# Performance work log

Hardware: AMD Instinct MI355X
Metric: run time of the kernel (lower is better)

The kernel has to match this reference:

```python
import jax, jax.numpy as jnp
import numpy as np

NUM_AUTHOR = 16604
NUM_PAPER = 12455
NUM_NODES = NUM_AUTHOR + NUM_PAPER  # 29059
EMBED_DIM = 300
B = 32768          # batch of query nodes
E = 1048576        # total neighbor edges (avg degree 32)


def setup_inputs() -> dict:
    key = jax.random.key(0)
    k1, k2, k3, k4, k5, k6 = jax.random.split(key, 6)
    nodes = jax.random.randint(k1, (B,), 0, NUM_NODES)
    seg = jnp.sort(jax.random.randint(k2, (E,), 0, B))
    neighbors = jax.random.randint(k3, (E,), 0, NUM_NODES)
    embeddings = jax.random.normal(k4, (NUM_NODES, EMBED_DIM), dtype=jnp.float32)
    # linear1: Linear(3*300 -> 300)
    lim = 1.0 / np.sqrt(3 * EMBED_DIM)
    W1 = jax.random.uniform(k5, (EMBED_DIM, 3 * EMBED_DIM), dtype=jnp.float32, minval=-lim, maxval=lim)
    b1 = jax.random.uniform(k6, (EMBED_DIM,), dtype=jnp.float32, minval=-lim, maxval=lim)
    return {"nodes": nodes, "seg": seg, "neighbors": neighbors,
            "embeddings": embeddings, "W1": W1, "b1": b1}


def reference(nodes, seg, neighbors, embeddings, W1, b1):
    # Gather neighbor embeddings: [E, D] (dominant memory traffic)
    nb_emb = embeddings[neighbors]
    # type_1 = same node type as the query node, type_2 = the other type
    same = (neighbors < NUM_AUTHOR) == (nodes[seg] < NUM_AUTHOR)  # [E] bool
    w1 = same.astype(nb_emb.dtype)[:, None]
    w2 = 1.0 - w1
    sum1 = jax.ops.segment_sum(nb_emb * w1, seg, num_segments=B)   # [B, D]
    sum2 = jax.ops.segment_sum(nb_emb * w2, seg, num_segments=B)
    cnt1 = jax.ops.segment_sum(w1[:, 0], seg, num_segments=B)[:, None]  # [B,1]
    cnt2 = jax.ops.segment_sum(w2[:, 0], seg, num_segments=B)[:, None]
    # mean pooling; empty type falls back to ones (as in the torch code)
    t1 = jnp.where(cnt1 > 0, sum1 / jnp.maximum(cnt1, 1.0), 1.0)
    t2 = jnp.where(cnt2 > 0, sum2 / jnp.maximum(cnt2, 1.0), 1.0)
    self_f = embeddings[nodes]  # [B, D]
    combined = jnp.concatenate([self_f, t1, t2], axis=-1)  # [B, 3D]
    return combined @ W1.T + b1  # [B, D]
```

## Files before the change

### kernel.cpp

```cpp
#include <hip/hip_runtime.h>
#include <hip/hip_bf16.h>

#define NUM_AUTHOR 16604
#define EMB_D      300
#define BQ         32768
#define NEDGE      1048576
#define KPAD 960
#define NPAD 320
#define DPAD 320
#define NNODES 29059

typedef __attribute__((ext_vector_type(8))) short bf16x8;
typedef __attribute__((ext_vector_type(4))) float f32x4;

__device__ __forceinline__ unsigned short f2bf(float f) {
  unsigned int u = __float_as_uint(f);
  u += 0x7fffu + ((u >> 16) & 1u);
  return (unsigned short)(u >> 16);
}

__device__ __forceinline__ void async_copy16(const void* g, void* lds_base) {
  __builtin_amdgcn_global_load_lds(
      (const __attribute__((address_space(1))) unsigned int*)g,
      (__attribute__((address_space(3))) unsigned int*)lds_base, 16, 0, 0);
}

__global__ void seg_bounds(const int* __restrict__ seg, int* __restrict__ start) {
  int i = blockIdx.x * 256 + threadIdx.x;
  if (i >= NEDGE) return;
  int s = seg[i];
  int prev = (i == 0) ? -1 : seg[i - 1];
  if (s != prev) {
    for (int b = prev + 1; b <= s; ++b) start[b] = i;
  }
  if (i == NEDGE - 1) {
    for (int b = s + 1; b <= BQ; ++b) start[b] = NEDGE;
  }
}

__global__ void prep_w(const float* __restrict__ W1,
                       unsigned short* __restrict__ Wt) {
  int i = blockIdx.x * 256 + threadIdx.x;
  if (i >= NPAD * KPAD) return;
  int n = i / KPAD, k = i % KPAD;
  int sec = k / 320, kk = k % 320;
  unsigned short v = 0;
  if (n < 300 && kk < 300) v = f2bf(W1[n * 900 + sec * 300 + kk]);
  Wt[i] = v;
}

__global__ void conv_emb(const float* __restrict__ emb,
                         unsigned short* __restrict__ embB) {
  int i = blockIdx.x * 256 + threadIdx.x;
  if (i >= NNODES * (DPAD / 2)) return;
  int r = i / (DPAD / 2), cu = i % (DPAD / 2);
  int c = 2 * cu;
  unsigned int lo = 0, hi = 0;
  if (c < EMB_D)     lo = f2bf(emb[(size_t)r * EMB_D + c]);
  if (c + 1 < EMB_D) hi = f2bf(emb[(size_t)r * EMB_D + c + 1]);
  ((unsigned int*)embB)[i] = lo | (hi << 16);
}

__device__ __forceinline__ void accum8(uint4 p, int b1,
                                       float* atot, float* a1) {
  unsigned int pk[4] = {p.x, p.y, p.z, p.w};
  float v[8];
  #pragma unroll
  for (int k = 0; k < 4; ++k) {
    v[2 * k]     = __uint_as_float(pk[k] << 16);
    v[2 * k + 1] = __uint_as_float(pk[k] & 0xffff0000u);
  }
  #pragma unroll
  for (int k = 0; k < 8; ++k) atot[k] += v[k];
  if (__builtin_amdgcn_readfirstlane(b1)) {
    #pragma unroll
    for (int k = 0; k < 8; ++k) a1[k] += v[k];
  }
}

__global__ __launch_bounds__(128) void pool(
    const int* __restrict__ nodes, const int* __restrict__ neighbors,
    const int* __restrict__ start, const unsigned short* __restrict__ embB,
    unsigned short* __restrict__ comb) {
  int b = blockIdx.x * 2 + (threadIdx.x >> 6);
  int l = threadIdx.x & 63;
  int s0 = start[b], s1 = start[b + 1];
  int node = nodes[b];
  int qa = (node < NUM_AUTHOR) ? 1 : 0;
  bool act = (l < 40);
  const unsigned short* ep = embB + 8 * l;

  float atot[8], a1[8];
  #pragma unroll
  for (int k = 0; k < 8; ++k) { atot[k] = 0.f; a1[k] = 0.f; }
  int c1 = 0;
  int rem = s1 - s0;

  for (int base = 0; base < rem; base += 64) {
    int cl = min(64, rem - base);
    int idx = neighbors[s0 + base + min(l, cl - 1)];
    int same = (((idx < NUM_AUTHOR) ? 1 : 0) == qa) ? 1 : 0;
    unsigned long long bal = __ballot(same != 0);
    unsigned long long msk = (cl >= 64) ? ~0ull : ((1ull << cl) - 1ull);
    c1 += __popcll(bal & msk);
    int off = idx * DPAD;

    int j2 = 0;
    for (; j2 + 4 <= cl; j2 += 4) {
      int o0 = __shfl(off, j2);
      int o1 = __shfl(off, j2 + 1);
      int o2 = __shfl(off, j2 + 2);
      int o3 = __shfl(off, j2 + 3);
      uint4 p0, p1, p2, p3;
      if (act) {
        p0 = *(const uint4*)(ep + o0);
        p1 = *(const uint4*)(ep + o1);
        p2 = *(const uint4*)(ep + o2);
        p3 = *(const uint4*)(ep + o3);
        accum8(p0, (int)((bal >> j2) & 1), atot, a1);
        accum8(p1, (int)((bal >> (j2 + 1)) & 1), atot, a1);
        accum8(p2, (int)((bal >> (j2 + 2)) & 1), atot, a1);
        accum8(p3, (int)((bal >> (j2 + 3)) & 1), atot, a1);
      }
    }
    for (; j2 < cl; ++j2) {
      int o = __shfl(off, j2);
      if (act) {
        uint4 p = *(const uint4*)(ep + o);
        accum8(p, (int)((bal >> j2) & 1), atot, a1);
      }
    }
  }

  int c2 = rem - c1;
  if (!act) return;

  uint4 selfv = *(const uint4*)(embB + (size_t)node * DPAD + 8 * l);
  float r1 = c1 ? 1.0f / (float)c1 : 0.0f;
  float r2 = c2 ? 1.0f / (float)c2 : 0.0f;
  unsigned int o1[4], o2[4];
  #pragma unroll
  for (int k = 0; k < 4; ++k) {
    float t1lo = c1 ? a1[2 * k] * r1 : 1.0f;
    float t1hi = c1 ? a1[2 * k + 1] * r1 : 1.0f;
    float t2lo = c2 ? (atot[2 * k] - a1[2 * k]) * r2 : 1.0f;
    float t2hi = c2 ? (atot[2 * k + 1] - a1[2 * k + 1]) * r2 : 1.0f;
    o1[k] = (unsigned int)f2bf(t1lo) | ((unsigned int)f2bf(t1hi) << 16);
    o2[k] = (unsigned int)f2bf(t2lo) | ((unsigned int)f2bf(t2hi) << 16);
  }
  uint4* crow = (uint4*)(comb + (size_t)b * KPAD);
  crow[l]      = selfv;
  crow[40 + l] = (uint4){o1[0], o1[1], o1[2], o1[3]};
  crow[80 + l] = (uint4){o2[0], o2[1], o2[2], o2[3]};
}

__global__ __launch_bounds__(128) void pool_f32(
    const int* __restrict__ nodes, const int* __restrict__ neighbors,
    const int* __restrict__ start, const float* __restrict__ emb,
    unsigned short* __restrict__ comb) {
  int b = blockIdx.x;
  int t = threadIdx.x;
  if (t >= 80) return;
  int s0 = start[b], s1 = start[b + 1];
  int node = nodes[b];
  int qa = (node < NUM_AUTHOR) ? 1 : 0;
  bool act = (t < 75);
  float a1x = 0.f, a1y = 0.f, a1z = 0.f, a1w = 0.f;
  float a2x = 0.f, a2y = 0.f, a2z = 0.f, a2w = 0.f;
  int c1 = 0;
  #pragma unroll 2
  for (int j = s0; j < s1; ++j) {
    int nb = neighbors[j];
    int fl = (((nb < NUM_AUTHOR) ? 1 : 0) == qa) ? 1 : 0;
    c1 += fl;
    if (act) {
      const float4 v = *(const float4*)(emb + (size_t)nb * EMB_D + 4 * t);
      float w = fl ? 1.0f : 0.0f;
      float u = 1.0f - w;
      a1x += w * v.x; a1y += w * v.y; a1z += w * v.z; a1w += w * v.w;
      a2x += u * v.x; a2y += u * v.y; a2z += u * v.z; a2w += u * v.w;
    }
  }
  int c2 = (s1 - s0) - c1;
  unsigned int ps0 = 0, ps1 = 0, p10 = 0, p11 = 0, p20 = 0, p21 = 0;
  if (act) {
    const float4 sv = *(const float4*)(emb + (size_t)node * EMB_D + 4 * t);
    float r1 = c1 ? 1.0f / (float)c1 : 0.0f;
    float r2 = c2 ? 1.0f / (float)c2 : 0.0f;
    float t1x = c1 ? a1x * r1 : 1.0f, t1y = c1 ? a1y * r1 : 1.0f;
    float t1z = c1 ? a1z * r1 : 1.0f, t1w = c1 ? a1w * r1 : 1.0f;
    float t2x = c2 ? a2x * r2 : 1.0f, t2y = c2 ? a2y * r2 : 1.0f;
    float t2z = c2 ? a2z * r2 : 1.0f, t2w = c2 ? a2w * r2 : 1.0f;
    ps0 = (unsigned int)f2bf(sv.x) | ((unsigned int)f2bf(sv.y) << 16);
    ps1 = (unsigned int)f2bf(sv.z) | ((unsigned int)f2bf(sv.w) << 16);
    p10 = (unsigned int)f2bf(t1x) | ((unsigned int)f2bf(t1y) << 16);
    p11 = (unsigned int)f2bf(t1z) | ((unsigned int)f2bf(t1w) << 16);
    p20 = (unsigned int)f2bf(t2x) | ((unsigned int)f2bf(t2y) << 16);
    p21 = (unsigned int)f2bf(t2z) | ((unsigned int)f2bf(t2w) << 16);
  }
  unsigned int* crow = (unsigned int*)(comb + (size_t)b * KPAD);
  crow[2 * t]       = ps0;  crow[2 * t + 1]       = ps1;
  crow[160 + 2 * t] = p10;  crow[160 + 2 * t + 1] = p11;
  crow[320 + 2 * t] = p20;  crow[320 + 2 * t + 1] = p21;
}

__global__ __launch_bounds__(256) void gemm(
    const unsigned short* __restrict__ A,
    const unsigned short* __restrict__ Bt,
    const float* __restrict__ b1,
    float* __restrict__ out) {
  __shared__ __align__(16) unsigned short As[128 * 32];
  __shared__ __align__(16) unsigned short Bs[160 * 32];

  int tid  = threadIdx.x;
  int lane = tid & 63;
  int w    = tid >> 6;
  int quad = lane >> 4;
  int l16  = lane & 15;
  int bm = blockIdx.x >> 1;
  int bn = blockIdx.x & 1;
  int wm = w >> 1, wn = w & 1;

  f32x4 acc[4][5];
  for (int i = 0; i < 4; ++i)
    for (int j = 0; j < 5; ++j)
      acc[i][j] = (f32x4){0.f, 0.f, 0.f, 0.f};

  const size_t Abase = (size_t)bm * 128 * KPAD;
  const size_t Bbase = (size_t)bn * 160 * KPAD;

  for (int kt = 0; kt < KPAD / 32; ++kt) {
    int k0 = kt * 32;
    __syncthreads();
    for (int c = w; c < 8; c += 4) {
      int flat = c * 64 + lane;
      int row = flat >> 2, kq = flat & 3;
      const unsigned short* g = A + Abase + (size_t)row * KPAD + k0 + kq * 8;
      async_copy16(g, (char*)As + c * 1024);
    }
    for (int c = w; c < 10; c += 4) {
      int flat = c * 64 + lane;
      int nrow = flat >> 2, kq = flat & 3;
      const unsigned short* g = Bt + Bbase + (size_t)nrow * KPAD + k0 + kq * 8;
      async_copy16(g, (char*)Bs + c * 1024);
    }
    __syncthreads();

    bf16x8 af[4], bf[5];
    for (int rt = 0; rt < 4; ++rt)
      af[rt] = *(const bf16x8*)&As[(wm * 64 + rt * 16 + l16) * 32 + quad * 8];
    for (int ct = 0; ct < 5; ++ct)
      bf[ct] = *(const bf16x8*)&Bs[(wn * 80 + ct * 16 + l16) * 32 + quad * 8];
    for (int rt = 0; rt < 4; ++rt)
      for (int ct = 0; ct < 5; ++ct)
        acc[rt][ct] = __builtin_amdgcn_mfma_f32_16x16x32_bf16(
            af[rt], bf[ct], acc[rt][ct], 0, 0, 0);
  }

  int m0 = bm * 128 + wm * 64;
  int n0 = bn * 160 + wn * 80;
  for (int ct = 0; ct < 5; ++ct) {
    int n = n0 + ct * 16 + l16;
    if (n >= 300) continue;
    float bias = b1[n];
    for (int rt = 0; rt < 4; ++rt) {
      int m = m0 + rt * 16 + quad * 4;
      for (int r = 0; r < 4; ++r)
        out[(size_t)(m + r) * 300 + n] = acc[rt][ct][r] + bias;
    }
  }
}

extern "C" void kernel_launch(void* const* d_in, const int* in_sizes, int n_in,
                              void* d_out, int out_size, void* d_ws, size_t ws_size,
                              hipStream_t stream) {
  const int* nodes     = (const int*)d_in[0];
  const int* seg       = (const int*)d_in[1];
  const int* neighbors = (const int*)d_in[2];
  const float* emb     = (const float*)d_in[3];
  const float* W1      = (const float*)d_in[4];
  const float* b1      = (const float*)d_in[5];
  float* out           = (float*)d_out;

  char* ws = (char*)d_ws;
  int* start           = (int*)ws;
  unsigned short* Wt   = (unsigned short*)(ws + 131584);
  unsigned short* comb = (unsigned short*)(ws + 746496);
  unsigned short* embB = (unsigned short*)(ws + 63661056);
  const size_t WS_NEEDED = 82258816;

  seg_bounds<<<NEDGE / 256, 256, 0, stream>>>(seg, start);
  prep_w<<<(NPAD * KPAD + 255) / 256, 256, 0, stream>>>(W1, Wt);
  if (ws_size >= WS_NEEDED) {
    conv_emb<<<(NNODES * (DPAD / 2) + 255) / 256, 256, 0, stream>>>(emb, embB);
    pool<<<BQ / 2, 128, 0, stream>>>(nodes, neighbors, start, embB, comb);
  } else {
    pool_f32<<<BQ, 128, 0, stream>>>(nodes, neighbors, start, emb, comb);
  }
  gemm<<<512, 256, 0, stream>>>(comb, Wt, b1, out);
}
```

Measured before the change: 232.5 us.

## Merge prep kernels into one launch, widen gather unroll, halve GEMM M-tile

Combines the segment-bounds, weight-conversion and embedding-conversion kernels into a single launch with block-range dispatch, removing two launch gaps. The pooling gather loop now issues eight neighbor-row loads before accumulating instead of four, for more memory-level parallelism. The GEMM M-tile drops from 128 to 64 rows, doubling the grid to 1024 blocks for better CU occupancy at the cost of re-reading the weight tile twice as often. The accumulators become float2 pairs, which is mostly cosmetic.

New measurement: 228.0 us. No clear change (-1.9%).

```diff
diff --git a/kernel.cpp b/kernel.cpp
--- a/kernel.cpp
+++ b/kernel.cpp
@@ -10,6 +10,10 @@
 #define DPAD 320
 #define NNODES 29059
 
+#define SEG_BLOCKS 4096
+#define PW_BLOCKS  1200
+#define CE_BLOCKS  18162
+
 typedef __attribute__((ext_vector_type(8))) short bf16x8;
 typedef __attribute__((ext_vector_type(4))) float f32x4;
 
@@ -25,56 +29,57 @@
       (__attribute__((address_space(3))) unsigned int*)lds_base, 16, 0, 0);
 }
 
-__global__ void seg_bounds(const int* __restrict__ seg, int* __restrict__ start) {
-  int i = blockIdx.x * 256 + threadIdx.x;
-  if (i >= NEDGE) return;
-  int s = seg[i];
-  int prev = (i == 0) ? -1 : seg[i - 1];
-  if (s != prev) {
-    for (int b = prev + 1; b <= s; ++b) start[b] = i;
-  }
-  if (i == NEDGE - 1) {
-    for (int b = s + 1; b <= BQ; ++b) start[b] = NEDGE;
-  }
-}
-
-__global__ void prep_w(const float* __restrict__ W1,
-                       unsigned short* __restrict__ Wt) {
-  int i = blockIdx.x * 256 + threadIdx.x;
-  if (i >= NPAD * KPAD) return;
-  int n = i / KPAD, k = i % KPAD;
-  int sec = k / 320, kk = k % 320;
-  unsigned short v = 0;
-  if (n < 300 && kk < 300) v = f2bf(W1[n * 900 + sec * 300 + kk]);
-  Wt[i] = v;
-}
-
-__global__ void conv_emb(const float* __restrict__ emb,
-                         unsigned short* __restrict__ embB) {
-  int i = blockIdx.x * 256 + threadIdx.x;
-  if (i >= NNODES * (DPAD / 2)) return;
-  int r = i / (DPAD / 2), cu = i % (DPAD / 2);
-  int c = 2 * cu;
-  unsigned int lo = 0, hi = 0;
-  if (c < EMB_D)     lo = f2bf(emb[(size_t)r * EMB_D + c]);
-  if (c + 1 < EMB_D) hi = f2bf(emb[(size_t)r * EMB_D + c + 1]);
-  ((unsigned int*)embB)[i] = lo | (hi << 16);
-}
-
-__device__ __forceinline__ void accum8(uint4 p, int b1,
-                                       float* atot, float* a1) {
+__global__ void prep_all(const int* __restrict__ seg, int* __restrict__ start,
+                         const float* __restrict__ W1, unsigned short* __restrict__ Wt,
+                         const float* __restrict__ emb, unsigned short* __restrict__ embB) {
+  int blk = blockIdx.x;
+  if (blk < SEG_BLOCKS) {
+    int i = blk * 256 + threadIdx.x;
+    int s = seg[i];
+    int prev = (i == 0) ? -1 : seg[i - 1];
+    if (s != prev) {
+      for (int b = prev + 1; b <= s; ++b) start[b] = i;
+    }
+    if (i == NEDGE - 1) {
+      for (int b = s + 1; b <= BQ; ++b) start[b] = NEDGE;
+    }
+  } else if (blk < SEG_BLOCKS + PW_BLOCKS) {
+    int i = (blk - SEG_BLOCKS) * 256 + threadIdx.x;
+    int n = i / KPAD, k = i % KPAD;
+    int sec = k / 320, kk = k % 320;
+    unsigned short v = 0;
+    if (n < 300 && kk < 300) v = f2bf(W1[n * 900 + sec * 300 + kk]);
+    Wt[i] = v;
+  } else {
+    int i = (blk - SEG_BLOCKS - PW_BLOCKS) * 256 + threadIdx.x;
+    if (i >= NNODES * (DPAD / 2)) return;
+    int r = i / (DPAD / 2), cu = i % (DPAD / 2);
+    int c = 2 * cu;
+    unsigned int lo = 0, hi = 0;
+    if (c < EMB_D)     lo = f2bf(emb[(size_t)r * EMB_D + c]);
+    if (c + 1 < EMB_D) hi = f2bf(emb[(size_t)r * EMB_D + c + 1]);
+    ((unsigned int*)embB)[i] = lo | (hi << 16);
+  }
+}
+
+__device__ __forceinline__ void accum8(uint4 p, int bit,
+                                       float2* atot, float2* a1) {
   unsigned int pk[4] = {p.x, p.y, p.z, p.w};
-  float v[8];
+  float2 v[4];
   #pragma unroll
   for (int k = 0; k < 4; ++k) {
-    v[2 * k]     = __uint_as_float(pk[k] << 16);
-    v[2 * k + 1] = __uint_as_float(pk[k] & 0xffff0000u);
+    v[k].x = __uint_as_float(pk[k] << 16);
+    v[k].y = __uint_as_float(pk[k] & 0xffff0000u);
   }
   #pragma unroll
-  for (int k = 0; k < 8; ++k) atot[k] += v[k];
-  if (__builtin_amdgcn_readfirstlane(b1)) {
+  for (int k = 0; k < 4; ++k) {
+    atot[k].x += v[k].x; atot[k].y += v[k].y;
+  }
+  if (__builtin_amdgcn_readfirstlane(bit)) {
     #pragma unroll
-    for (int k = 0; k < 8; ++k) a1[k] += v[k];
+    for (int k = 0; k < 4; ++k) {
+      a1[k].x += v[k].x; a1[k].y += v[k].y;
+    }
   }
 }
 
@@ -90,9 +95,12 @@
   bool act = (l < 40);
   const unsigned short* ep = embB + 8 * l;
 
-  float atot[8], a1[8];
+  float2 atot[4], a1[4];
   #pragma unroll
-  for (int k = 0; k < 8; ++k) { atot[k] = 0.f; a1[k] = 0.f; }
+  for (int k = 0; k < 4; ++k) {
+    atot[k] = make_float2(0.f, 0.f);
+    a1[k]   = make_float2(0.f, 0.f);
+  }
   int c1 = 0;
   int rem = s1 - s0;
 
@@ -106,21 +114,17 @@
     int off = idx * DPAD;
 
     int j2 = 0;
-    for (; j2 + 4 <= cl; j2 += 4) {
-      int o0 = __shfl(off, j2);
-      int o1 = __shfl(off, j2 + 1);
-      int o2 = __shfl(off, j2 + 2);
-      int o3 = __shfl(off, j2 + 3);
-      uint4 p0, p1, p2, p3;
+    for (; j2 + 8 <= cl; j2 += 8) {
+      int o[8];
+      #pragma unroll
+      for (int q = 0; q < 8; ++q) o[q] = __shfl(off, j2 + q);
       if (act) {
-        p0 = *(const uint4*)(ep + o0);
-        p1 = *(const uint4*)(ep + o1);
-        p2 = *(const uint4*)(ep + o2);
-        p3 = *(const uint4*)(ep + o3);
-        accum8(p0, (int)((bal >> j2) & 1), atot, a1);
-        accum8(p1, (int)((bal >> (j2 + 1)) & 1), atot, a1);
-        accum8(p2, (int)((bal >> (j2 + 2)) & 1), atot, a1);
-        accum8(p3, (int)((bal >> (j2 + 3)) & 1), atot, a1);
+        uint4 p[8];
+        #pragma unroll
+        for (int q = 0; q < 8; ++q) p[q] = *(const uint4*)(ep + o[q]);
+        #pragma unroll
+        for (int q = 0; q < 8; ++q)
+          accum8(p[q], (int)((bal >> (j2 + q)) & 1), atot, a1);
       }
     }
     for (; j2 < cl; ++j2) {
@@ -141,10 +145,10 @@
   unsigned int o1[4], o2[4];
   #pragma unroll
   for (int k = 0; k < 4; ++k) {
-    float t1lo = c1 ? a1[2 * k] * r1 : 1.0f;
-    float t1hi = c1 ? a1[2 * k + 1] * r1 : 1.0f;
-    float t2lo = c2 ? (atot[2 * k] - a1[2 * k]) * r2 : 1.0f;
-    float t2hi = c2 ? (atot[2 * k + 1] - a1[2 * k + 1]) * r2 : 1.0f;
+    float t1lo = c1 ? a1[k].x * r1 : 1.0f;
+    float t1hi = c1 ? a1[k].y * r1 : 1.0f;
+    float t2lo = c2 ? (atot[k].x - a1[k].x) * r2 : 1.0f;
+    float t2hi = c2 ? (atot[k].y - a1[k].y) * r2 : 1.0f;
     o1[k] = (unsigned int)f2bf(t1lo) | ((unsigned int)f2bf(t1hi) << 16);
     o2[k] = (unsigned int)f2bf(t2lo) | ((unsigned int)f2bf(t2hi) << 16);
   }
@@ -152,6 +156,73 @@
   crow[l]      = selfv;
   crow[40 + l] = (uint4){o1[0], o1[1], o1[2], o1[3]};
   crow[80 + l] = (uint4){o2[0], o2[1], o2[2], o2[3]};
+}
+
+__global__ __launch_bounds__(256) void gemm(
+    const unsigned short* __restrict__ A,
+    const unsigned short* __restrict__ Bt,
+    const float* __restrict__ b1,
+    float* __restrict__ out) {
+  __shared__ __align__(16) unsigned short As[64 * 32];
+  __shared__ __align__(16) unsigned short Bs[160 * 32];
+
+  int tid  = threadIdx.x;
+  int lane = tid & 63;
+  int w    = tid >> 6;
+  int quad = lane >> 4;
+  int l16  = lane & 15;
+  int bm = blockIdx.x >> 1;
+  int bn = blockIdx.x & 1;
+  int wm = w >> 1, wn = w & 1;
+
+  f32x4 acc[2][5];
+  for (int i = 0; i < 2; ++i)
+    for (int j = 0; j < 5; ++j)
+      acc[i][j] = (f32x4){0.f, 0.f, 0.f, 0.f};
+
+  const size_t Abase = (size_t)bm * 64 * KPAD;
+  const size_t Bbase = (size_t)bn * 160 * KPAD;
+
+  for (int kt = 0; kt < KPAD / 32; ++kt) {
+    int k0 = kt * 32;
+    __syncthreads();
+    for (int c = w; c < 4; c += 4) {
+      int flat = c * 64 + lane;
+      int row = flat >> 2, kq = flat & 3;
+      const unsigned short* g = A + Abase + (size_t)row * KPAD + k0 + kq * 8;
+      async_copy16(g, (char*)As + c * 1024);
+    }
+    for (int c = w; c < 10; c += 4) {
+      int flat = c * 64 + lane;
+      int nrow = flat >> 2, kq = flat & 3;
+      const unsigned short* g = Bt + Bbase + (size_t)nrow * KPAD + k0 + kq * 8;
+      async_copy16(g, (char*)Bs + c * 1024);
+    }
+    __syncthreads();
+
+    bf16x8 af[2], bf[5];
+    for (int rt = 0; rt < 2; ++rt)
+      af[rt] = *(const bf16x8*)&As[(wm * 32 + rt * 16 + l16) * 32 + quad * 8];
+    for (int ct = 0; ct < 5; ++ct)
+      bf[ct] = *(const bf16x8*)&Bs[(wn * 80 + ct * 16 + l16) * 32 + quad * 8];
+    for (int rt = 0; rt < 2; ++rt)
+      for (int ct = 0; ct < 5; ++ct)
+        acc[rt][ct] = __builtin_amdgcn_mfma_f32_16x16x32_bf16(
+            af[rt], bf[ct], acc[rt][ct], 0, 0, 0);
+  }
+
+  int m0 = bm * 64 + wm * 32;
+  int n0 = bn * 160 + wn * 80;
+  for (int ct = 0; ct < 5; ++ct) {
+    int n = n0 + ct * 16 + l16;
+    if (n >= 300) continue;
+    float bias = b1[n];
+    for (int rt = 0; rt < 2; ++rt) {
+      int m = m0 + rt * 16 + quad * 4;
+      for (int r = 0; r < 4; ++r)
+        out[(size_t)(m + r) * 300 + n] = acc[rt][ct][r] + bias;
+    }
+  }
 }
 
 __global__ __launch_bounds__(128) void pool_f32(
@@ -204,71 +275,22 @@
   crow[320 + 2 * t] = p20;  crow[320 + 2 * t + 1] = p21;
 }
 
-__global__ __launch_bounds__(256) void gemm(
-    const unsigned short* __restrict__ A,
-    const unsigned short* __restrict__ Bt,
-    const float* __restrict__ b1,
-    float* __restrict__ out) {
-  __shared__ __align__(16) unsigned short As[128 * 32];
-  __shared__ __align__(16) unsigned short Bs[160 * 32];
-
-  int tid  = threadIdx.x;
-  int lane = tid & 63;
-  int w    = tid >> 6;
-  int quad = lane >> 4;
-  int l16  = lane & 15;
-  int bm = blockIdx.x >> 1;
-  int bn = blockIdx.x & 1;
-  int wm = w >> 1, wn = w & 1;
-
-  f32x4 acc[4][5];
-  for (int i = 0; i < 4; ++i)
-    for (int j = 0; j < 5; ++j)
-      acc[i][j] = (f32x4){0.f, 0.f, 0.f, 0.f};
-
-  const size_t Abase = (size_t)bm * 128 * KPAD;
-  const size_t Bbase = (size_t)bn * 160 * KPAD;
-
-  for (int kt = 0; kt < KPAD / 32; ++kt) {
-    int k0 = kt * 32;
-    __syncthreads();
-    for (int c = w; c < 8; c += 4) {
-      int flat = c * 64 + lane;
-      int row = flat >> 2, kq = flat & 3;
-      const unsigned short* g = A + Abase + (size_t)row * KPAD + k0 + kq * 8;
-      async_copy16(g, (char*)As + c * 1024);
-    }
-    for (int c = w; c < 10; c += 4) {
-      int flat = c * 64 + lane;
-      int nrow = flat >> 2, kq = flat & 3;
-      const unsigned short* g = Bt + Bbase + (size_t)nrow * KPAD + k0 + kq * 8;
-      async_copy16(g, (char*)Bs + c * 1024);
-    }
-    __syncthreads();
-
-    bf16x8 af[4], bf[5];
-    for (int rt = 0; rt < 4; ++rt)
-      af[rt] = *(const bf16x8*)&As[(wm * 64 + rt * 16 + l16) * 32 + quad * 8];
-    for (int ct = 0; ct < 5; ++ct)
-      bf[ct] = *(const bf16x8*)&Bs[(wn * 80 + ct * 16 + l16) * 32 + quad * 8];
-    for (int rt = 0; rt < 4; ++rt)
-      for (int ct = 0; ct < 5; ++ct)
-        acc[rt][ct] = __builtin_amdgcn_mfma_f32_16x16x32_bf16(
-            af[rt], bf[ct], acc[rt][ct], 0, 0, 0);
-  }
-
-  int m0 = bm * 128 + wm * 64;
-  int n0 = bn * 160 + wn * 80;
-  for (int ct = 0; ct < 5; ++ct) {
-    int n = n0 + ct * 16 + l16;
-    if (n >= 300) continue;
-    float bias = b1[n];
-    for (int rt = 0; rt < 4; ++rt) {
-      int m = m0 + rt * 16 + quad * 4;
-      for (int r = 0; r < 4; ++r)
-        out[(size_t)(m + r) * 300 + n] = acc[rt][ct][r] + bias;
-    }
-  }
+__global__ void seg_bounds_only(const int* __restrict__ seg, int* __restrict__ start) {
+  int i = blockIdx.x * 256 + threadIdx.x;
+  if (i >= NEDGE) return;
+  int s = seg[i];
+  int prev = (i == 0) ? -1 : seg[i - 1];
+  if (s != prev) for (int b = prev + 1; b <= s; ++b) start[b] = i;
+  if (i == NEDGE - 1) for (int b = s + 1; b <= BQ; ++b) start[b] = NEDGE;
+}
+__global__ void prep_w_only(const float* __restrict__ W1, unsigned short* __restrict__ Wt) {
+  int i = blockIdx.x * 256 + threadIdx.x;
+  if (i >= NPAD * KPAD) return;
+  int n = i / KPAD, k = i % KPAD;
+  int sec = k / 320, kk = k % 320;
+  unsigned short v = 0;
+  if (n < 300 && kk < 300) v = f2bf(W1[n * 900 + sec * 300 + kk]);
+  Wt[i] = v;
 }
 
 extern "C" void kernel_launch(void* const* d_in, const int* in_sizes, int n_in,
@@ -289,13 +311,14 @@
   unsigned short* embB = (unsigned short*)(ws + 63661056);
   const size_t WS_NEEDED = 82258816;
 
-  seg_bounds<<<NEDGE / 256, 256, 0, stream>>>(seg, start);
-  prep_w<<<(NPAD * KPAD + 255) / 256, 256, 0, stream>>>(W1, Wt);
   if (ws_size >= WS_NEEDED) {
-    conv_emb<<<(NNODES * (DPAD / 2) + 255) / 256, 256, 0, stream>>>(emb, embB);
+    prep_all<<<SEG_BLOCKS + PW_BLOCKS + CE_BLOCKS, 256, 0, stream>>>(
+        seg, start, W1, Wt, emb, embB);
     pool<<<BQ / 2, 128, 0, stream>>>(nodes, neighbors, start, embB, comb);
   } else {
+    seg_bounds_only<<<SEG_BLOCKS, 256, 0, stream>>>(seg, start);
+    prep_w_only<<<PW_BLOCKS, 256, 0, stream>>>(W1, Wt);
     pool_f32<<<BQ, 128, 0, stream>>>(nodes, neighbors, start, emb, comb);
   }
-  gemm<<<512, 256, 0, stream>>>(comb, Wt, b1, out);
-}
+  gemm<<<1024, 256, 0, stream>>>(comb, Wt, b1, out);
+}
```
